# Kernel tuning notes

Hardware: AMD Instinct MI355X
Metric: run time of the kernel (lower is better)

## Reference

```python
import jax, jax.numpy as jnp
import numpy as np

N = 8000      # nodes (spatial spots)
E = 40000     # directed edges (kNN graph, avg degree 5)
DIN = 1024    # input_dim
H = 3         # heads
C = 1024      # hidden_dim per head
NCLS = 460    # n_classes
NCEN = 100    # centroid count (pass-through only)
NEG_SLOPE = 0.2


def setup_inputs() -> dict:
    key = jax.random.key(0)
    ks = jax.random.split(key, 12)
    s_in = 1.0 / np.sqrt(DIN)   # glorot-ish scale for 1024 fan-in
    s_h = 1.0 / np.sqrt(C)
    return {
        'x': jax.random.normal(ks[0], (N, DIN), jnp.float32),
        'edge_index': jax.random.randint(ks[1], (E, 2), 0, N),  # [E,2] (src,dst)
        'Wl': jax.random.normal(ks[2], (DIN, H * C), jnp.float32) * s_in,
        'bl': jnp.zeros((H * C,), jnp.float32),
        'Wr': jax.random.normal(ks[3], (DIN, H * C), jnp.float32) * s_in,
        'br': jnp.zeros((H * C,), jnp.float32),
        'att': jax.random.normal(ks[4], (H, C), jnp.float32) * s_h,
        'bias': jnp.zeros((C,), jnp.float32),
        'Wf': jax.random.normal(ks[5], (C, NCLS), jnp.float32) * s_h,
        'bf': jnp.zeros((NCLS,), jnp.float32),
        'exps': jax.random.uniform(ks[6], (N, NCLS), jnp.float32),
        'exps_c': jax.random.uniform(ks[7], (NCEN, NCLS), jnp.float32),
    }


def reference(x, edge_index, Wl, bl, Wr, br, att, bias, Wf, bf, exps, exps_c):
    n = x.shape[0]
    h_, c_ = att.shape
    # PyG GATv2Conv default add_self_loops=True
    loops = jnp.arange(n)
    src = jnp.concatenate([edge_index[:, 0], loops])
    dst = jnp.concatenate([edge_index[:, 1], loops])
    # lin_l / lin_r projections -> [N,H,C]
    xl = (x @ Wl + bl).reshape(n, h_, c_)
    xr = (x @ Wr + br).reshape(n, h_, c_)
    # GATv2 edge scores: a^T LeakyReLU(x_l[src] + x_r[dst])  -> [Etot,H]
    s = jax.nn.leaky_relu(xl[src] + xr[dst], NEG_SLOPE)
    e = jnp.einsum('ehc,hc->eh', s, att)
    # segment softmax over incoming edges per dst node (PyG softmax: +1e-16)
    m = jax.lax.stop_gradient(jax.ops.segment_max(e, dst, num_segments=n))
    a = jnp.exp(e - m[dst])
    denom = jax.ops.segment_sum(a, dst, num_segments=n)
    alpha = a / (denom[dst] + 1e-16)
    # weighted scatter-add of source messages
    out = jax.ops.segment_sum(alpha[:, :, None] * xl[src], dst, num_segments=n)
    # concat=False -> mean over heads, then conv bias
    out = out.mean(axis=1) + bias
    # fc + row softmax
    h = jax.nn.softmax(out @ Wf + bf, axis=-1)
    return h
```

## Files before the change

kernel.cpp:

```cpp
#include <hip/hip_runtime.h>

#define NNODES 8000
#define MPAD   8064
#define NEDGES 40000
#define ETOT   (NEDGES + NNODES)
#define DIN    1024
#define NH     3
#define CH     1024
#define HC     (NH * CH)
#define NTOT   (2 * HC)
#define NCLS   460
#define NCLS_P 512
#define NEG    0.2f

typedef _Float16 h8 __attribute__((ext_vector_type(8)));
typedef _Float16 h4v __attribute__((ext_vector_type(4)));
typedef float    f4 __attribute__((ext_vector_type(4)));

#define GLOAD16(g, l) \
    __builtin_amdgcn_global_load_lds((const __attribute__((address_space(1))) void*)(g), \
                                     (__attribute__((address_space(3))) void*)(l), 16, 0, 0)

__global__ __launch_bounds__(256)
void fp16_pad_convert(const float* __restrict__ in, _Float16* __restrict__ out,
                      int rows_in, int rows_out, int cols)
{
    size_t i4 = (size_t)blockIdx.x * 256 + threadIdx.x;
    size_t tot = ((size_t)rows_out * cols) >> 2;
    if (i4 >= tot) return;
    size_t e = i4 << 2;
    int row = (int)(e / cols);
    float vx = 0.f, vy = 0.f, vz = 0.f, vw = 0.f;
    if (row < rows_in) {
        float4 v = *(const float4*)(in + e);
        vx = v.x; vy = v.y; vz = v.z; vw = v.w;
    }
    h4v o = { (_Float16)vx, (_Float16)vy, (_Float16)vz, (_Float16)vw };
    *(h4v*)(out + e) = o;
}

__global__ __launch_bounds__(256)
void transpose_to_fp16(const float* __restrict__ W, _Float16* __restrict__ Wt,
                       int K, int Ncols, int rowOff)
{
    __shared__ float tile[32][33];
    int n0 = blockIdx.x * 32, k0 = blockIdx.y * 32;
    int tx = threadIdx.x, ty = threadIdx.y;
    #pragma unroll
    for (int i = 0; i < 4; ++i) {
        int k = k0 + ty + i * 8;
        int n = n0 + tx;
        tile[ty + i * 8][tx] = (n < Ncols) ? W[(size_t)k * Ncols + n] : 0.f;
    }
    __syncthreads();
    #pragma unroll
    for (int i = 0; i < 4; ++i) {
        int n = n0 + ty + i * 8;
        int k = k0 + tx;
        Wt[(size_t)(rowOff + n) * K + k] = (_Float16)tile[tx][ty + i * 8];
    }
}

__global__ __launch_bounds__(256)
void bias_pack(const float* __restrict__ bl, const float* __restrict__ br,
               const float* __restrict__ bf, const float* __restrict__ att,
               float* __restrict__ b1, float* __restrict__ b2, _Float16* __restrict__ atth)
{
    int i = blockIdx.x * 256 + threadIdx.x;
    if (i < HC) { b1[i] = bl[i]; b1[HC + i] = br[i]; atth[i] = (_Float16)att[i]; }
    if (i < NCLS_P) b2[i] = (i < NCLS) ? bf[i] : 0.f;
}

__global__ __launch_bounds__(256)
void csr_count(const int* __restrict__ ei, int* __restrict__ cnt)
{
    int e = blockIdx.x * 256 + threadIdx.x;
    if (e >= ETOT) return;
    int dst = (e < NEDGES) ? ei[2 * e + 1] : (e - NEDGES);
    atomicAdd(&cnt[dst], 1);
}

__global__ __launch_bounds__(1024)
void csr_scan(const int* __restrict__ cnt, int* __restrict__ rofs)
{
    __shared__ int s[1024];
    int t = threadIdx.x;
    int base = t * 8;
    int local[8];
    int sum = 0;
    #pragma unroll
    for (int i = 0; i < 8; ++i) {
        local[i] = sum;
        sum += (base + i < NNODES) ? cnt[base + i] : 0;
    }
    s[t] = sum;
    __syncthreads();
    for (int off = 1; off < 1024; off <<= 1) {
        int v = (t >= off) ? s[t - off] : 0;
        __syncthreads();
        if (t >= off) s[t] += v;
        __syncthreads();
    }
    int pre = (t > 0) ? s[t - 1] : 0;
    #pragma unroll
    for (int i = 0; i < 8; ++i)
        if (base + i < NNODES) rofs[base + i] = pre + local[i];
}

__global__ __launch_bounds__(256)
void csr_fill(const int* __restrict__ ei, const int* __restrict__ rofs,
              int* __restrict__ cursor, int* __restrict__ csr_src)
{
    int e = blockIdx.x * 256 + threadIdx.x;
    if (e >= ETOT) return;
    int src, dst;
    if (e < NEDGES) { src = ei[2 * e]; dst = ei[2 * e + 1]; }
    else            { src = dst = e - NEDGES; }
    int pos = rofs[dst] + atomicAdd(&cursor[dst], 1);
    csr_src[pos] = src;
}

__global__ __launch_bounds__(256, 4)
void gemm_f16(const _Float16* __restrict__ A, const _Float16* __restrict__ Bt,
              const float* __restrict__ biasN,
              float* __restrict__ C32, _Float16* __restrict__ C16,
              int N, int K)
{
    __shared__ __align__(16) _Float16 sA[128 * 32];
    __shared__ __align__(16) _Float16 sB[128 * 32];

    int nwg = gridDim.x;
    int orig = blockIdx.x;
    int q = nwg >> 3, r = nwg & 7;
    int xcd = orig & 7, idx = orig >> 3;
    int wg = (xcd < r ? xcd * (q + 1) : r * (q + 1) + (xcd - r) * q) + idx;
    int nbx = N >> 7;
    int bm = wg / nbx, bn = wg - bm * nbx;
    int m0 = bm << 7, n0 = bn << 7;

    const int t = threadIdx.x;
    const int lane = t & 63, w = t >> 6;
    const int wr = (w >> 1) << 6, wc = (w & 1) << 6;

    f4 acc[4][4];
    f4 zero = { 0.f, 0.f, 0.f, 0.f };
    #pragma unroll
    for (int i = 0; i < 4; ++i)
        #pragma unroll
        for (int j = 0; j < 4; ++j) acc[i][j] = zero;

    const int lr = lane >> 2, lk = lane & 3;
    const _Float16* gA = A  + (size_t)(m0 + w * 16 + lr) * K + lk * 8;
    const _Float16* gB = Bt + (size_t)(n0 + w * 16 + lr) * K + lk * 8;
    _Float16* lA0 = &sA[w * 512];
    _Float16* lA1 = &sA[2048 + w * 512];
    _Float16* lB0 = &sB[w * 512];
    _Float16* lB1 = &sB[2048 + w * 512];
    const size_t seg = (size_t)64 * K;

    const int nk = K >> 5;
    for (int s = 0; s < nk; ++s) {
        const int ko = s << 5;
        GLOAD16(gA + ko,       lA0);
        GLOAD16(gA + seg + ko, lA1);
        GLOAD16(gB + ko,       lB0);
        GLOAD16(gB + seg + ko, lB1);
        __syncthreads();
        const int ks = lane >> 4;
        h8 bh[4];
        #pragma unroll
        for (int nj = 0; nj < 4; ++nj)
            bh[nj] = *(const h8*)&sB[(wc + nj * 16 + (lane & 15)) * 32 + ks * 8];
        #pragma unroll
        for (int mi = 0; mi < 4; ++mi) {
            h8 ah = *(const h8*)&sA[(wr + mi * 16 + (lane & 15)) * 32 + ks * 8];
            #pragma unroll
            for (int nj = 0; nj < 4; ++nj)
                acc[mi][nj] = __builtin_amdgcn_mfma_f32_16x16x32_f16(ah, bh[nj], acc[mi][nj], 0, 0, 0);
        }
        __syncthreads();
    }

    #pragma unroll
    for (int mi = 0; mi < 4; ++mi) {
        #pragma unroll
        for (int nj = 0; nj < 4; ++nj) {
            int col  = n0 + wc + nj * 16 + (lane & 15);
            int rowb = m0 + wr + mi * 16 + ((lane >> 4) << 2);
            float b = biasN[col];
            #pragma unroll
            for (int rg = 0; rg < 4; ++rg) {
                float v = acc[mi][nj][rg] + b;
                size_t off = (size_t)(rowb + rg) * N + col;
                if (C32) C32[off] = v;
                else     C16[off] = (_Float16)v;
            }
        }
    }
}

__global__ __launch_bounds__(256)
void edge_fused(const _Float16* __restrict__ xlr, const int* __restrict__ rofs,
                const int* __restrict__ cnt, const int* __restrict__ csr_src,
                const _Float16* __restrict__ atth, const float* __restrict__ bias,
                _Float16* __restrict__ o2h)
{
    const int wid = threadIdx.x >> 6;
    const int dst = (blockIdx.x << 2) + wid;
    const int l   = threadIdx.x & 63;
    const int cb0 = l << 3, cb1 = 512 + (l << 3);

    h8 xr[3][2], at[3][2];
    #pragma unroll
    for (int h = 0; h < 3; ++h) {
        const _Float16* pr = xlr + (size_t)dst * NTOT + HC + h * CH;
        xr[h][0] = *(const h8*)(pr + cb0);
        xr[h][1] = *(const h8*)(pr + cb1);
        at[h][0] = *(const h8*)(atth + h * CH + cb0);
        at[h][1] = *(const h8*)(atth + h * CH + cb1);
    }

    const int beg = rofs[dst];
    const int num = cnt[dst];

    float m[3] = { -3.4e38f, -3.4e38f, -3.4e38f };
    float d[3] = { 0.f, 0.f, 0.f };
    float acc[3][2][8] = {};

    for (int i = 0; i < num; ++i) {
        int src = csr_src[beg + i];
        const _Float16* ps = xlr + (size_t)src * NTOT;
        h8 xv[3][2];
        #pragma unroll
        for (int h = 0; h < 3; ++h) {
            xv[h][0] = *(const h8*)(ps + h * CH + cb0);
            xv[h][1] = *(const h8*)(ps + h * CH + cb1);
        }
        #pragma unroll
        for (int h = 0; h < 3; ++h) {
            float s = 0.f;
            #pragma unroll
            for (int b = 0; b < 2; ++b)
                #pragma unroll
                for (int j = 0; j < 8; ++j) {
                    float z = (float)xv[h][b][j] + (float)xr[h][b][j];
                    z = z > 0.f ? z : NEG * z;
                    s = fmaf((float)at[h][b][j], z, s);
                }
            #pragma unroll
            for (int off = 32; off > 0; off >>= 1) s += __shfl_xor(s, off);
            float nm = fmaxf(m[h], s);
            float rs = __expf(m[h] - nm);
            float wt = __expf(s - nm);
            d[h] = d[h] * rs + wt;
            #pragma unroll
            for (int b = 0; b < 2; ++b)
                #pragma unroll
                for (int j = 0; j < 8; ++j)
                    acc[h][b][j] = fmaf(wt, (float)xv[h][b][j], acc[h][b][j] * rs);
            m[h] = nm;
        }
    }

    float inv0 = 1.f / (d[0] + 1e-16f) * (1.f / 3.f);
    float inv1 = 1.f / (d[1] + 1e-16f) * (1.f / 3.f);
    float inv2 = 1.f / (d[2] + 1e-16f) * (1.f / 3.f);
    #pragma unroll
    for (int b = 0; b < 2; ++b) {
        int c = b ? cb1 : cb0;
        h8 o;
        #pragma unroll
        for (int j = 0; j < 8; ++j) {
            float v = acc[0][b][j] * inv0 + acc[1][b][j] * inv1 + acc[2][b][j] * inv2
                    + bias[c + j];
            o[j] = (_Float16)v;
        }
        *(h8*)(o2h + (size_t)dst * CH + c) = o;
    }
}

__global__ __launch_bounds__(64)
void row_softmax(const float* __restrict__ logits, float* __restrict__ out)
{
    const int r = blockIdx.x;
    const int lane = threadIdx.x;
    const float* row = logits + (size_t)r * NCLS_P;
    float v[8];
    float mx = -3.4e38f;
    #pragma unroll
    for (int i = 0; i < 8; ++i) {
        int c = lane + i * 64;
        v[i] = (c < NCLS) ? row[c] : -3.4e38f;
        mx = fmaxf(mx, v[i]);
    }
    #pragma unroll
    for (int off = 32; off > 0; off >>= 1) mx = fmaxf(mx, __shfl_xor(mx, off));
    float s = 0.f;
    #pragma unroll
    for (int i = 0; i < 8; ++i) {
        int c = lane + i * 64;
        float ev = (c < NCLS) ? expf(v[i] - mx) : 0.f;
        v[i] = ev;
        s += ev;
    }
    #pragma unroll
    for (int off = 32; off > 0; off >>= 1) s += __shfl_xor(s, off);
    float inv = 1.f / s;
    #pragma unroll
    for (int i = 0; i < 8; ++i) {
        int c = lane + i * 64;
        if (c < NCLS) out[(size_t)r * NCLS + c] = v[i] * inv;
    }
}

extern "C" void kernel_launch(void* const* d_in, const int* in_sizes, int n_in,
                              void* d_out, int out_size, void* d_ws, size_t ws_size,
                              hipStream_t stream)
{
    (void)in_sizes; (void)n_in; (void)out_size; (void)ws_size;

    const float* x    = (const float*)d_in[0];
    const int*   ei   = (const int*)  d_in[1];
    const float* Wl   = (const float*)d_in[2];
    const float* bl   = (const float*)d_in[3];
    const float* Wr   = (const float*)d_in[4];
    const float* br   = (const float*)d_in[5];
    const float* att  = (const float*)d_in[6];
    const float* bias = (const float*)d_in[7];
    const float* Wf   = (const float*)d_in[8];
    const float* bf   = (const float*)d_in[9];

    char* base = (char*)d_ws;
    _Float16* xh      = (_Float16*)(base);
    _Float16* BtW     = (_Float16*)(base + 16515072);
    _Float16* Wft     = (_Float16*)(base + 29097984);
    float*    biasC1  = (float*)   (base + 30146560);
    float*    biasC2  = (float*)   (base + 30171136);
    _Float16* atth    = (_Float16*)(base + 30173184);
    int*      cnt     = (int*)     (base + 30179328);
    int*      cursor  = (int*)     (base + 30211328);
    int*      rofs    = (int*)     (base + 30243328);
    int*      csr_src = (int*)     (base + 30275328);
    _Float16* o2h     = (_Float16*)(base + 30467328);
    float*    logits  = (float*)   (base + 46982400);
    _Float16* xlr     = (_Float16*)(base + 63497472);

    hipMemsetAsync(cnt, 0, 64000, stream);
    hipMemsetAsync(o2h + (size_t)NNODES * CH, 0, (size_t)(MPAD - NNODES) * CH * 2, stream);

    fp16_pad_convert<<<(MPAD * DIN / 4 + 255) / 256, 256, 0, stream>>>(
        x, xh, NNODES, MPAD, DIN);

    transpose_to_fp16<<<dim3(HC / 32, DIN / 32), dim3(32, 8), 0, stream>>>(Wl, BtW, DIN, HC, 0);
    transpose_to_fp16<<<dim3(HC / 32, DIN / 32), dim3(32, 8), 0, stream>>>(Wr, BtW, DIN, HC, HC);
    transpose_to_fp16<<<dim3(NCLS_P / 32, DIN / 32), dim3(32, 8), 0, stream>>>(Wf, Wft, DIN, NCLS, 0);

    bias_pack<<<(HC + 255) / 256, 256, 0, stream>>>(bl, br, bf, att, biasC1, biasC2, atth);

    csr_count<<<(ETOT + 255) / 256, 256, 0, stream>>>(ei, cnt);
    csr_scan<<<1, 1024, 0, stream>>>(cnt, rofs);
    csr_fill<<<(ETOT + 255) / 256, 256, 0, stream>>>(ei, rofs, cursor, csr_src);

    gemm_f16<<<(NTOT / 128) * (MPAD / 128), 256, 0, stream>>>(
        xh, BtW, biasC1, nullptr, xlr, NTOT, DIN);

    edge_fused<<<NNODES / 4, 256, 0, stream>>>(xlr, rofs, cnt, csr_src, atth, bias, o2h);

    gemm_f16<<<(NCLS_P / 128) * (MPAD / 128), 256, 0, stream>>>(
        o2h, Wft, biasC2, logits, nullptr, NCLS_P, DIN);

    row_softmax<<<NNODES, 64, 0, stream>>>(logits, (float*)d_out);
}
```

Baseline: 421.4 us.

## Use 256x256-tile eight-wave pipelined GEMM for the projection matmul

Adds a new fp16 MFMA GEMM kernel with 256x256 tiles, 512 threads and a 128KB double-buffered LDS stage. It interleaves global-to-LDS loads with MFMA phases and raises wave priority during the math. It replaces the 128x128 GEMM for the large x@[Wl|Wr] projection, and the M padding grows to 8192 to fit the tile. The aim is more data reuse per tile and better overlap of loads with compute. The cost is lower occupancy, extra padded rows, and a fixed XCD remap that assumes the grid divides by 8.

After: 422.8 us. About the same (+0.3%).

```diff
diff --git a/kernel.cpp b/kernel.cpp
--- a/kernel.cpp
+++ b/kernel.cpp
@@ -1,7 +1,7 @@
 #include <hip/hip_runtime.h>
 
 #define NNODES 8000
-#define MPAD   8064
+#define MPAD   8192
 #define NEDGES 40000
 #define ETOT   (NEDGES + NNODES)
 #define DIN    1024
@@ -120,6 +120,125 @@
     csr_src[pos] = src;
 }
 
+__global__ __launch_bounds__(512, 2)
+void gemm256_f16(const _Float16* __restrict__ A, const _Float16* __restrict__ Bt,
+                 const float* __restrict__ biasN, _Float16* __restrict__ C16,
+                 int N, int K)
+{
+    __shared__ __align__(16) _Float16 lds[65536];
+
+    int nwg = gridDim.x;
+    int orig = blockIdx.x;
+    int cpx = nwg >> 3;
+    int wg = (orig & 7) * cpx + (orig >> 3);
+    int nbx = N >> 8;
+    int bm = wg / nbx, bn = wg - bm * nbx;
+    int m0 = bm << 8, n0 = bn << 8;
+
+    const int t = threadIdx.x;
+    const int lane = t & 63;
+    const int w = t >> 6;
+    const int wm = w >> 2;
+    const int wn = w & 3;
+
+    const int sRow = lane >> 3;
+    const int sCol = (lane & 7) << 3;
+    const int seg0 = w << 1;
+
+    const int l15 = lane & 15;
+    const int kl8 = (lane >> 4) << 3;
+
+    f4 acc[8][4];
+    f4 zero = { 0.f, 0.f, 0.f, 0.f };
+    #pragma unroll
+    for (int i = 0; i < 8; ++i)
+        #pragma unroll
+        for (int j = 0; j < 4; ++j) acc[i][j] = zero;
+
+    auto STAGE_A = [&](int kt, int h, int b) {
+        const _Float16* src = A + (size_t)(m0 + h * 128 + seg0 * 8 + sRow) * K + kt * 64 + sCol;
+        int dst = b * 32768 + h * 8192 + seg0 * 512;
+        GLOAD16(src, &lds[dst]);
+        GLOAD16(src + (size_t)8 * K, &lds[dst + 512]);
+    };
+    auto STAGE_B = [&](int kt, int h, int b) {
+        const _Float16* src = Bt + (size_t)(n0 + h * 128 + seg0 * 8 + sRow) * K + kt * 64 + sCol;
+        int dst = b * 32768 + 16384 + h * 8192 + seg0 * 512;
+        GLOAD16(src, &lds[dst]);
+        GLOAD16(src + (size_t)8 * K, &lds[dst + 512]);
+    };
+
+    h8 bfr[4][2];
+    const int aBase = wm * 128 + l15;
+    const int bBase = wn * 64 + l15;
+
+#define DS_A(fi, ks2, q, b) (*(const h8*)&lds[(b)*32768 + (aBase + (q)*32 + (fi)*16)*64 + (ks2)*32 + kl8])
+#define DS_B(nf, ks2, b)    (*(const h8*)&lds[(b)*32768 + 16384 + (bBase + (nf)*16)*64 + (ks2)*32 + kl8])
+
+#define PHASE(b, q, STAGE_STMT, VMEND)                                                            \
+    {                                                                                             \
+        h8 a00 = DS_A(0, 0, q, b), a01 = DS_A(0, 1, q, b);                                        \
+        h8 a10 = DS_A(1, 0, q, b), a11 = DS_A(1, 1, q, b);                                        \
+        if ((q) == 0) {                                                                           \
+            _Pragma("unroll")                                                                     \
+            for (int nf = 0; nf < 4; ++nf) {                                                      \
+                bfr[nf][0] = DS_B(nf, 0, b);                                                      \
+                bfr[nf][1] = DS_B(nf, 1, b);                                                      \
+            }                                                                                     \
+        }                                                                                         \
+        STAGE_STMT;                                                                               \
+        __builtin_amdgcn_s_barrier();                                                             \
+        asm volatile("s_waitcnt lgkmcnt(0)" ::: "memory");                                        \
+        __builtin_amdgcn_sched_barrier(0);                                                        \
+        __builtin_amdgcn_s_setprio(1);                                                            \
+        _Pragma("unroll")                                                                         \
+        for (int nf = 0; nf < 4; ++nf) {                                                          \
+            acc[(q)*2+0][nf] = __builtin_amdgcn_mfma_f32_16x16x32_f16(a00, bfr[nf][0], acc[(q)*2+0][nf], 0, 0, 0); \
+            acc[(q)*2+0][nf] = __builtin_amdgcn_mfma_f32_16x16x32_f16(a01, bfr[nf][1], acc[(q)*2+0][nf], 0, 0, 0); \
+            acc[(q)*2+1][nf] = __builtin_amdgcn_mfma_f32_16x16x32_f16(a10, bfr[nf][0], acc[(q)*2+1][nf], 0, 0, 0); \
+            acc[(q)*2+1][nf] = __builtin_amdgcn_mfma_f32_16x16x32_f16(a11, bfr[nf][1], acc[(q)*2+1][nf], 0, 0, 0); \
+        }                                                                                         \
+        __builtin_amdgcn_s_setprio(0);                                                            \
+        if (VMEND) asm volatile("s_waitcnt vmcnt(4)" ::: "memory");                               \
+        __builtin_amdgcn_s_barrier();                                                             \
+    }
+
+    STAGE_A(0, 0, 0); STAGE_A(0, 1, 0);
+    STAGE_B(0, 0, 0); STAGE_B(0, 1, 0);
+    STAGE_B(1, 0, 1); STAGE_B(1, 1, 1);
+    asm volatile("s_waitcnt vmcnt(4)" ::: "memory");
+    __builtin_amdgcn_s_barrier();
+
+    const int NKT = K >> 6;
+    for (int kt = 0; kt < NKT; kt += 2) {
+        PHASE(0, 0, STAGE_A(kt + 1, 0, 1), false);
+        PHASE(0, 1, STAGE_A(kt + 1, 1, 1), false);
+        PHASE(0, 2, STAGE_B(kt + 2, 0, 0), false);
+        PHASE(0, 3, STAGE_B(kt + 2, 1, 0), true);
+        PHASE(1, 0, STAGE_A(kt + 2, 0, 0), false);
+        PHASE(1, 1, STAGE_A(kt + 2, 1, 0), false);
+        PHASE(1, 2, STAGE_B(kt + 3, 0, 1), false);
+        PHASE(1, 3, STAGE_B(kt + 3, 1, 1), true);
+    }
+
+#undef PHASE
+#undef DS_A
+#undef DS_B
+
+    #pragma unroll
+    for (int mf = 0; mf < 8; ++mf) {
+        int row0 = m0 + wm * 128 + mf * 16 + ((lane >> 4) << 2);
+        #pragma unroll
+        for (int nf = 0; nf < 4; ++nf) {
+            int col = n0 + wn * 64 + nf * 16 + l15;
+            float bb = biasN[col];
+            #pragma unroll
+            for (int rg = 0; rg < 4; ++rg)
+                C16[(size_t)(row0 + rg) * N + col] = (_Float16)(acc[mf][nf][rg] + bb);
+        }
+    }
+}
+
 __global__ __launch_bounds__(256, 4)
 void gemm_f16(const _Float16* __restrict__ A, const _Float16* __restrict__ Bt,
               const float* __restrict__ biasN,
@@ -332,18 +451,18 @@
 
     char* base = (char*)d_ws;
     _Float16* xh      = (_Float16*)(base);
-    _Float16* BtW     = (_Float16*)(base + 16515072);
-    _Float16* Wft     = (_Float16*)(base + 29097984);
-    float*    biasC1  = (float*)   (base + 30146560);
-    float*    biasC2  = (float*)   (base + 30171136);
-    _Float16* atth    = (_Float16*)(base + 30173184);
-    int*      cnt     = (int*)     (base + 30179328);
-    int*      cursor  = (int*)     (base + 30211328);
-    int*      rofs    = (int*)     (base + 30243328);
-    int*      csr_src = (int*)     (base + 30275328);
-    _Float16* o2h     = (_Float16*)(base + 30467328);
-    float*    logits  = (float*)   (base + 46982400);
-    _Float16* xlr     = (_Float16*)(base + 63497472);
+    _Float16* BtW     = (_Float16*)(base + 16777216);
+    _Float16* Wft     = (_Float16*)(base + 29360128);
+    float*    biasC1  = (float*)   (base + 30408704);
+    float*    biasC2  = (float*)   (base + 30433280);
+    _Float16* atth    = (_Float16*)(base + 30435328);
+    int*      cnt     = (int*)     (base + 30441472);
+    int*      cursor  = (int*)     (base + 30473472);
+    int*      rofs    = (int*)     (base + 30505472);
+    int*      csr_src = (int*)     (base + 30537472);
+    _Float16* o2h     = (_Float16*)(base + 30729472);
+    float*    logits  = (float*)   (base + 47506688);
+    _Float16* xlr     = (_Float16*)(base + 64283904);
 
     hipMemsetAsync(cnt, 0, 64000, stream);
     hipMemsetAsync(o2h + (size_t)NNODES * CH, 0, (size_t)(MPAD - NNODES) * CH * 2, stream);
@@ -361,8 +480,8 @@
     csr_scan<<<1, 1024, 0, stream>>>(cnt, rofs);
     csr_fill<<<(ETOT + 255) / 256, 256, 0, stream>>>(ei, rofs, cursor, csr_src);
 
-    gemm_f16<<<(NTOT / 128) * (MPAD / 128), 256, 0, stream>>>(
-        xh, BtW, biasC1, nullptr, xlr, NTOT, DIN);
+    gemm256_f16<<<(MPAD / 256) * (NTOT / 256), 512, 0, stream>>>(
+        xh, BtW, biasC1, xlr, NTOT, DIN);
 
     edge_fused<<<NNODES / 4, 256, 0, stream>>>(xlr, rofs, cnt, csr_src, atth, bias, o2h);
 
```
